# Kernel tuning notes

Hardware: AMD Instinct MI355X
Metric: run time of the kernel (lower is better)

The kernel has to match this reference:

```python
import jax, jax.numpy as jnp
import numpy as np

NUM_HEADS = 16

def setup_inputs() -> dict:
    key = jax.random.key(0)
    ks = jax.random.split(key, 5)
    b, c, w, h = 2, 1024, 48, 48
    sc = 0.02
    return {
        "x": jax.random.normal(ks[0], (b, c, w, h), jnp.float32),
        "Wqkv": jax.random.normal(ks[1], (3 * c, c), jnp.float32) * sc,
        "bqkv": jax.random.normal(ks[2], (3 * c,), jnp.float32) * sc,
        "Wo": jax.random.normal(ks[3], (c, c), jnp.float32) * sc,
        "bo": jax.random.normal(ks[4], (c,), jnp.float32) * sc,
    }

def reference(x, Wqkv, bqkv, Wo, bo):
    b, c, w, h = x.shape
    n = NUM_HEADS
    hd = c // n
    s = w * h
    # [b,c,w,h] -> tokens [b, s, c]
    xs = x.transpose(0, 2, 3, 1).reshape(b, s, c)
    qkv = xs @ Wqkv.T + bqkv                       # [b, s, 3c]
    # rearrange 'b s (three n hd) -> three b n s hd'
    qkv = qkv.reshape(b, s, 3, n, hd).transpose(2, 0, 3, 1, 4)
    q, k, v = qkv[0], qkv[1], qkv[2]               # [b, n, s, hd]
    score = jnp.einsum('bnqh,bnkh->bnqk', q, k) / jnp.sqrt(jnp.float32(hd))
    # module uses a soft causal mask: subtract 10000 above the diagonal
    mask = 10000.0 * jnp.triu(jnp.ones((s, s), dtype=score.dtype), k=1)
    attn = jax.nn.softmax(score - mask, axis=-1)   # [b, n, s, s]
    z = jnp.einsum('bnqk,bnkh->bqnh', attn, v).reshape(b, s, c)
    out = z @ Wo.T + bo                            # [b, s, c]
    return out.reshape(b, w, h, c).transpose(0, 3, 1, 2)
```

## Files before the change

### kernel.cpp

```cpp
#include <hip/hip_runtime.h>

typedef __bf16 bf16;
typedef __bf16 bf16x8 __attribute__((ext_vector_type(8)));
typedef float floatx4 __attribute__((ext_vector_type(4)));

static constexpr int S = 2304;
static constexpr int C = 1024;
static constexpr int NHEAD = 16;
static constexpr int HDIM = 64;
static constexpr int BATCH = 2;
static constexpr float QSCALE = 0.18033688011112042f;
static constexpr int QSPLIT = 18;
static constexpr int NACC = S - QSPLIT * 64;

__global__ __launch_bounds__(256) void k_zero(float4* __restrict__ p, int n4) {
  int i = blockIdx.x * 256 + threadIdx.x;
  if (i < n4) p[i] = float4{0.f, 0.f, 0.f, 0.f};
}

__global__ __launch_bounds__(256) void k_convert(const float* __restrict__ src,
                                                 bf16* __restrict__ dst, int n8) {
  int i = blockIdx.x * 256 + threadIdx.x;
  if (i >= n8) return;
  float4 a = *(const float4*)(src + (size_t)i * 8);
  float4 b = *(const float4*)(src + (size_t)i * 8 + 4);
  bf16x8 o;
  o[0] = (bf16)a.x; o[1] = (bf16)a.y; o[2] = (bf16)a.z; o[3] = (bf16)a.w;
  o[4] = (bf16)b.x; o[5] = (bf16)b.y; o[6] = (bf16)b.z; o[7] = (bf16)b.w;
  *(bf16x8*)(dst + (size_t)i * 8) = o;
}

__global__ __launch_bounds__(256) void k_transpose(const float* __restrict__ x,
                                                   bf16* __restrict__ xs) {
  __shared__ bf16 T[64 * 72];
  int c0 = blockIdx.x * 64, t0 = blockIdx.y * 64, b = blockIdx.z;
  int tid = threadIdx.x;
  const float* xb = x + (size_t)b * C * S;
#pragma unroll
  for (int it = 0; it < 4; ++it) {
    int idx = it * 256 + tid;
    int rc = idx >> 4, t4 = idx & 15;
    float4 v = *(const float4*)(xb + (size_t)(c0 + rc) * S + t0 + t4 * 4);
    T[(t4 * 4 + 0) * 72 + rc] = (bf16)v.x;
    T[(t4 * 4 + 1) * 72 + rc] = (bf16)v.y;
    T[(t4 * 4 + 2) * 72 + rc] = (bf16)v.z;
    T[(t4 * 4 + 3) * 72 + rc] = (bf16)v.w;
  }
  __syncthreads();
  bf16* xsb = xs + (size_t)b * S * C;
#pragma unroll
  for (int it = 0; it < 2; ++it) {
    int idx = it * 256 + tid;
    int rt = idx >> 3, c8 = idx & 7;
    bf16x8 v;
#pragma unroll
    for (int i = 0; i < 8; ++i) v[i] = T[rt * 72 + c8 * 8 + i];
    *(bf16x8*)(xsb + (size_t)(t0 + rt) * C + c0 + c8 * 8) = v;
  }
}

__device__ __forceinline__ void g2l16(const bf16* g, bf16* l) {
  __builtin_amdgcn_global_load_lds(
      (const __attribute__((address_space(1))) void*)g,
      (__attribute__((address_space(3))) void*)l, 16, 0, 0);
}

template <int EPI>
__global__ __launch_bounds__(256) void k_gemm_bt(const bf16* __restrict__ A,
                                                 const bf16* __restrict__ Bt,
                                                 const float* __restrict__ bias,
                                                 bf16* __restrict__ q,
                                                 bf16* __restrict__ k,
                                                 bf16* __restrict__ v,
                                                 float* __restrict__ outf) {
  constexpr int K = C;
  __shared__ bf16 As[128 * 64];
  __shared__ bf16 Bs[128 * 64];
  int tid = threadIdx.x;
  int w = tid >> 6, lane = tid & 63, ln = lane & 15, quad = lane >> 4;
  int m0 = blockIdx.y * 128, n0 = blockIdx.x * 128;
  int moff = (w >> 1) * 64, noff = (w & 1) * 64;
  floatx4 acc[4][4] = {};

  int sr[4], sc[4];
#pragma unroll
  for (int it = 0; it < 4; ++it) {
    int L = (it * 4 + w) * 64 + lane;
    sr[it] = L >> 3;
    sc[it] = (L & 7) ^ (sr[it] & 7);
  }

  for (int k0 = 0; k0 < K; k0 += 64) {
    __syncthreads();
#pragma unroll
    for (int it = 0; it < 4; ++it) {
      int cb = (it * 4 + w) * 64;
      g2l16(A + (size_t)(m0 + sr[it]) * K + k0 + sc[it] * 8, As + cb * 8);
      g2l16(Bt + (size_t)(n0 + sr[it]) * K + k0 + sc[it] * 8, Bs + cb * 8);
    }
    __syncthreads();
#pragma unroll
    for (int t = 0; t < 2; ++t) {
      bf16x8 af[4], bfr[4];
#pragma unroll
      for (int i = 0; i < 4; ++i) {
        int ra = moff + i * 16 + ln;
        af[i]  = *(const bf16x8*)(As + ra * 64 + (((t * 4 + quad) ^ (ra & 7))) * 8);
        int rb = noff + i * 16 + ln;
        bfr[i] = *(const bf16x8*)(Bs + rb * 64 + (((t * 4 + quad) ^ (rb & 7))) * 8);
      }
#pragma unroll
      for (int im = 0; im < 4; ++im)
#pragma unroll
        for (int in = 0; in < 4; ++in)
          acc[im][in] = __builtin_amdgcn_mfma_f32_16x16x32_bf16(
              af[im], bfr[in], acc[im][in], 0, 0, 0);
    }
  }

  int bidx = (m0 >= S) ? 1 : 0;
  if (EPI == 0) {
#pragma unroll
    for (int in = 0; in < 4; ++in) {
      int j = n0 + noff + in * 16 + ln;
      float bv = bias[j];
      int three = j >> 10;
      int head = (j >> 6) & 15;
      int hdi = j & 63;
#pragma unroll
      for (int im = 0; im < 4; ++im) {
        int mbase = m0 + moff + im * 16 + quad * 4;
        int tb = mbase - bidx * S;
        if (three == 2) {
          union { ushort4 u; bf16 h[4]; } P;
#pragma unroll
          for (int r = 0; r < 4; ++r) P.h[r] = (bf16)(acc[im][in][r] + bv);
          *(ushort4*)(v + ((size_t)(bidx * NHEAD + head) * HDIM + hdi) * S + tb) = P.u;
        } else if (three == 0) {
          bf16* dst = q + ((size_t)(bidx * NHEAD + head) * S + tb) * HDIM + hdi;
#pragma unroll
          for (int r = 0; r < 4; ++r)
            dst[(size_t)r * HDIM] = (bf16)((acc[im][in][r] + bv) * QSCALE);
        } else {
          bf16* dst = k + ((size_t)(bidx * NHEAD + head) * S + tb) * HDIM + hdi;
#pragma unroll
          for (int r = 0; r < 4; ++r) dst[(size_t)r * HDIM] = (bf16)(acc[im][in][r] + bv);
        }
      }
    }
  } else {
#pragma unroll
    for (int in = 0; in < 4; ++in) {
      int co = n0 + noff + in * 16 + ln;
      float bv = bias[co];
#pragma unroll
      for (int im = 0; im < 4; ++im) {
        int mbase = m0 + moff + im * 16 + quad * 4;
        int tb = mbase - bidx * S;
        float4 st;
        st.x = acc[im][in][0] + bv;
        st.y = acc[im][in][1] + bv;
        st.z = acc[im][in][2] + bv;
        st.w = acc[im][in][3] + bv;
        *(float4*)(outf + ((size_t)bidx * C + co) * S + tb) = st;
      }
    }
  }
}

__global__ __launch_bounds__(512) void k_attn_part(const bf16* __restrict__ Qg,
                                                   const bf16* __restrict__ Kg,
                                                   const bf16* __restrict__ Vtg,
                                                   bf16* __restrict__ z,
                                                   float* __restrict__ Oacc,
                                                   float* __restrict__ Lacc) {
  __shared__ bf16 Ks[2][64 * 64];
  __shared__ bf16 Vs[2][64 * 64];
  __shared__ bf16 Pt[128 * 64];
  int i = blockIdx.x;
  int xcd = i & 7, j = i >> 3;
  int grp = j / 27, r = j % 27;
  int bh = xcd + 8 * grp;
  int qi, lo, hi;
  bool single = (r >= 18);
  if (!single) {
    qi = 17 - (r >> 1);
    lo = (r & 1) * (qi + 1);
    hi = lo + qi + 1;
  } else {
    qi = 26 - r;
    lo = 0;
    hi = 2 * qi + 2;
  }
  int b = bh >> 4, h = bh & 15;
  int tid = threadIdx.x;
  int w = tid >> 6, lane = tid & 63, ln = lane & 15, quad = lane >> 4;
  int q0 = qi * 128;
  int qw = q0 + w * 16;
  int qg = qw + ln;
  int ktd = qw >> 6;

  const bf16* kb = Kg + (size_t)bh * S * HDIM;
  const bf16* vb = Vtg + (size_t)bh * HDIM * S;

  int s_row = tid >> 3, s_c8 = tid & 7;
  int s_cs = s_c8 ^ (s_row & 7);
  size_t kOff = (size_t)s_row * HDIM + s_cs * 8;
  size_t vOff = (size_t)s_row * S + s_cs * 8;

  const bf16* qb = Qg + ((size_t)bh * S + qg) * HDIM + quad * 8;
  bf16x8 qf0 = *(const bf16x8*)qb;
  bf16x8 qf1 = *(const bf16x8*)(qb + 32);

  float lsum = 0.f;
  floatx4 o_acc[4] = {};

  int prow = w * 16 + ln;
  int psw = ln & 7;
  bf16* ptw = Pt + prow * 64 + (quad & 1) * 4;
  const bf16* ptr = Pt + prow * 64;
  int qloc = (w & 3) * 16 + ln;

  const bf16* kb0 = kb + (size_t)lo * 64 * HDIM;
  const bf16* vb0 = vb + (size_t)lo * 64;
  g2l16(kb0 + kOff, Ks[0] + tid * 8);
  g2l16(vb0 + vOff, Vs[0] + tid * 8);

  const bf16* kbn = kb0 + (size_t)64 * HDIM;
  const bf16* vbn = vb0 + 64;

#pragma unroll 1
  for (int kt = lo; kt < hi; ++kt) {
    int cur = (kt - lo) & 1;
    __syncthreads();

    if (kt + 1 < hi) {
      g2l16(kbn + kOff, Ks[1 - cur] + tid * 8);
      g2l16(vbn + vOff, Vs[1 - cur] + tid * 8);
      kbn += (size_t)64 * HDIM;
      vbn += 64;
    }

    if (kt > ktd) continue;

    floatx4 s_acc[4] = {};
#pragma unroll
    for (int kf = 0; kf < 4; ++kf) {
      int row = kf * 16 + ln;
      int sw = row & 7;
      bf16x8 k0 = *(const bf16x8*)(Ks[cur] + row * 64 + (sw ^ quad) * 8);
      bf16x8 k1 = *(const bf16x8*)(Ks[cur] + row * 64 + ((4 ^ sw) ^ quad) * 8);
      s_acc[kf] = __builtin_amdgcn_mfma_f32_16x16x32_bf16(k0, qf0, s_acc[kf], 0, 0, 0);
      s_acc[kf] = __builtin_amdgcn_mfma_f32_16x16x32_bf16(k1, qf1, s_acc[kf], 0, 0, 0);
    }

    if (kt < ktd) {
#pragma unroll
      for (int kf = 0; kf < 4; ++kf) {
        union { ushort4 u; bf16 hh[4]; } P;
#pragma unroll
        for (int rr = 0; rr < 4; ++rr) {
          float pv = exp2f(s_acc[kf][rr]);
          lsum += pv;
          P.hh[rr] = (bf16)pv;
        }
        *(ushort4*)(ptw + (((kf * 2 + (quad >> 1)) ^ psw)) * 8) = P.u;
      }
    } else {
#pragma unroll
      for (int kf = 0; kf < 4; ++kf) {
        union { ushort4 u; bf16 hh[4]; } P;
#pragma unroll
        for (int rr = 0; rr < 4; ++rr) {
          int kl = kf * 16 + quad * 4 + rr;
          float pv = (kl > qloc) ? 0.f : exp2f(s_acc[kf][rr]);
          lsum += pv;
          P.hh[rr] = (bf16)pv;
        }
        *(ushort4*)(ptw + (((kf * 2 + (quad >> 1)) ^ psw)) * 8) = P.u;
      }
    }

#pragma unroll
    for (int t = 0; t < 2; ++t) {
      bf16x8 pf = *(const bf16x8*)(ptr + (((t * 4 + quad) ^ psw)) * 8);
#pragma unroll
      for (int hf = 0; hf < 4; ++hf) {
        int row = hf * 16 + ln;
        int sw = row & 7;
        bf16x8 vf = *(const bf16x8*)(Vs[cur] + row * 64 + (((t * 4 + quad) ^ sw)) * 8);
        o_acc[hf] = __builtin_amdgcn_mfma_f32_16x16x32_bf16(vf, pf, o_acc[hf], 0, 0, 0);
      }
    }
  }

  lsum += __shfl_xor(lsum, 16);
  lsum += __shfl_xor(lsum, 32);

  if (single) {
    float inv = 1.f / lsum;
    bf16* dst = z + ((size_t)b * S + qg) * C + h * HDIM + quad * 4;
#pragma unroll
    for (int hf = 0; hf < 4; ++hf) {
      union { ushort4 u; bf16 hh[4]; } P;
#pragma unroll
      for (int rr = 0; rr < 4; ++rr) P.hh[rr] = (bf16)(o_acc[hf][rr] * inv);
      *(ushort4*)(dst + hf * 16) = P.u;
    }
  } else {
    int qa = qg - QSPLIT * 64;
    if (lane < 16) atomicAdd(&Lacc[bh * NACC + qa], lsum);
#pragma unroll
    for (int hf = 0; hf < 4; ++hf)
#pragma unroll
      for (int rr = 0; rr < 4; ++rr)
        atomicAdd(&Oacc[((size_t)bh * 64 + hf * 16 + quad * 4 + rr) * NACC + qa],
                  o_acc[hf][rr]);
  }
}

__global__ __launch_bounds__(256) void k_norm(const float* __restrict__ Oacc,
                                              const float* __restrict__ Lacc,
                                              bf16* __restrict__ z) {
  __shared__ float T[64 * 65];
  int qt = blockIdx.x, bh = blockIdx.y;
  int b = bh >> 4, h = bh & 15;
  int qrel0 = qt * 64;
  int q0 = QSPLIT * 64 + qrel0;
  int tid = threadIdx.x;
  int q4 = (tid & 15) * 4, hd0 = tid >> 4;
  float4 lv = *(const float4*)(Lacc + bh * NACC + qrel0 + q4);
  float inv0 = 1.f / lv.x, inv1 = 1.f / lv.y, inv2 = 1.f / lv.z, inv3 = 1.f / lv.w;
#pragma unroll
  for (int hf = 0; hf < 4; ++hf) {
    int hd = hf * 16 + hd0;
    float4 v = *(const float4*)(Oacc + ((size_t)bh * 64 + hd) * NACC + qrel0 + q4);
    T[(q4 + 0) * 65 + hd] = v.x * inv0;
    T[(q4 + 1) * 65 + hd] = v.y * inv1;
    T[(q4 + 2) * 65 + hd] = v.z * inv2;
    T[(q4 + 3) * 65 + hd] = v.w * inv3;
  }
  __syncthreads();
#pragma unroll
  for (int it = 0; it < 2; ++it) {
    int idx = it * 256 + tid;
    int qq = idx >> 3, c8 = idx & 7;
    bf16x8 o;
#pragma unroll
    for (int k = 0; k < 8; ++k) o[k] = (bf16)T[qq * 65 + c8 * 8 + k];
    *(bf16x8*)(z + ((size_t)b * S + q0 + qq) * C + h * HDIM + c8 * 8) = o;
  }
}

extern "C" void kernel_launch(void* const* d_in, const int* in_sizes, int n_in,
                              void* d_out, int out_size, void* d_ws, size_t ws_size,
                              hipStream_t stream) {
  const float* x    = (const float*)d_in[0];
  const float* Wqkv = (const float*)d_in[1];
  const float* bqkv = (const float*)d_in[2];
  const float* Wo   = (const float*)d_in[3];
  const float* bo   = (const float*)d_in[4];
  float* out = (float*)d_out;

  bf16* ws = (bf16*)d_ws;
  const size_t tok = (size_t)BATCH * S * C;
  bf16* xs   = ws;
  bf16* Qg   = ws + tok;
  bf16* Kg   = ws + 2 * tok;
  bf16* Vtg  = ws + 3 * tok;
  bf16* Wqb  = ws + 4 * tok;
  bf16* Wob  = Wqb + (size_t)3 * C * C;
  float* Oacc = (float*)(Wob + (size_t)C * C);
  float* Lacc = Oacc + (size_t)32 * 64 * NACC;
  bf16* z    = xs;

  k_zero<<<2340, 256, 0, stream>>>((float4*)Oacc, 599040);
  k_convert<<<(3 * C * C / 8 + 255) / 256, 256, 0, stream>>>(Wqkv, Wqb, 3 * C * C / 8);
  k_convert<<<(C * C / 8 + 255) / 256, 256, 0, stream>>>(Wo, Wob, C * C / 8);
  k_transpose<<<dim3(C / 64, S / 64, BATCH), 256, 0, stream>>>(x, xs);
  k_gemm_bt<0><<<dim3(3 * C / 128, BATCH * S / 128), 256, 0, stream>>>(
      xs, Wqb, bqkv, Qg, Kg, Vtg, nullptr);
  k_attn_part<<<dim3(864), 512, 0, stream>>>(Qg, Kg, Vtg, z, Oacc, Lacc);
  k_norm<<<dim3(18, 32), 256, 0, stream>>>(Oacc, Lacc, z);
  k_gemm_bt<1><<<dim3(C / 128, BATCH * S / 128), 256, 0, stream>>>(
      z, Wob, bo, nullptr, nullptr, nullptr, out);
}
```

Before: 216.4 us.

## Switch attention to 32x32 MFMA with register-resident P via permlane swap

Rewrites the attention inner loop to use 32x32x16 bf16 MFMAs with 4 waves of 32 query rows each instead of 8 waves of 16 rows. The softmax probabilities are packed with v_cvt_pk_bf16_f32 and rearranged across lanes with v_permlane32_swap, so P goes straight into the PV MFMA operand without the LDS round trip and its shared buffer. It also adds s_setprio around the MFMA phases. The cost is higher register pressure per wave and fewer waves per block to hide latency.

```diff
diff --git a/kernel.cpp b/kernel.cpp
--- a/kernel.cpp
+++ b/kernel.cpp
@@ -3,6 +3,7 @@
 typedef __bf16 bf16;
 typedef __bf16 bf16x8 __attribute__((ext_vector_type(8)));
 typedef float floatx4 __attribute__((ext_vector_type(4)));
+typedef float floatx16 __attribute__((ext_vector_type(16)));
 
 static constexpr int S = 2304;
 static constexpr int C = 1024;
@@ -63,6 +64,16 @@
   __builtin_amdgcn_global_load_lds(
       (const __attribute__((address_space(1))) void*)g,
       (__attribute__((address_space(3))) void*)l, 16, 0, 0);
+}
+
+__device__ __forceinline__ unsigned cvtpk(float a, float b) {
+  unsigned r;
+  asm("v_cvt_pk_bf16_f32 %0, %1, %2" : "=v"(r) : "v"(a), "v"(b));
+  return r;
+}
+
+__device__ __forceinline__ void pl32(unsigned& a, unsigned& b) {
+  asm("v_permlane32_swap_b32 %0, %1" : "+v"(a), "+v"(b));
 }
 
 template <int EPI>
@@ -168,7 +179,7 @@
   }
 }
 
-__global__ __launch_bounds__(512) void k_attn_part(const bf16* __restrict__ Qg,
+__global__ __launch_bounds__(256) void k_attn_part(const bf16* __restrict__ Qg,
                                                    const bf16* __restrict__ Kg,
                                                    const bf16* __restrict__ Vtg,
                                                    bf16* __restrict__ z,
@@ -176,7 +187,6 @@
                                                    float* __restrict__ Lacc) {
   __shared__ bf16 Ks[2][64 * 64];
   __shared__ bf16 Vs[2][64 * 64];
-  __shared__ bf16 Pt[128 * 64];
   int i = blockIdx.x;
   int xcd = i & 7, j = i >> 3;
   int grp = j / 27, r = j % 27;
@@ -194,40 +204,42 @@
   }
   int b = bh >> 4, h = bh & 15;
   int tid = threadIdx.x;
-  int w = tid >> 6, lane = tid & 63, ln = lane & 15, quad = lane >> 4;
+  int w = tid >> 6, lane = tid & 63;
+  int ql = lane & 31, hw = lane >> 5;
   int q0 = qi * 128;
-  int qw = q0 + w * 16;
-  int qg = qw + ln;
+  int qw = q0 + w * 32;
+  int qg = qw + ql;
   int ktd = qw >> 6;
 
   const bf16* kb = Kg + (size_t)bh * S * HDIM;
   const bf16* vb = Vtg + (size_t)bh * HDIM * S;
 
-  int s_row = tid >> 3, s_c8 = tid & 7;
-  int s_cs = s_c8 ^ (s_row & 7);
-  size_t kOff = (size_t)s_row * HDIM + s_cs * 8;
-  size_t vOff = (size_t)s_row * S + s_cs * 8;
-
-  const bf16* qb = Qg + ((size_t)bh * S + qg) * HDIM + quad * 8;
-  bf16x8 qf0 = *(const bf16x8*)qb;
-  bf16x8 qf1 = *(const bf16x8*)(qb + 32);
+  int s_row = tid >> 3;
+  int s_c8 = (tid & 7) ^ (s_row & 7);
+  size_t kOff1 = (size_t)s_row * HDIM + s_c8 * 8;
+  size_t kOff2 = kOff1 + (size_t)32 * HDIM;
+  size_t vOff1 = (size_t)s_row * S + s_c8 * 8;
+  size_t vOff2 = vOff1 + (size_t)32 * S;
+
+  const bf16* qb = Qg + ((size_t)bh * S + qg) * HDIM + hw * 8;
+  bf16x8 qf[4];
+#pragma unroll
+  for (int c = 0; c < 4; ++c) qf[c] = *(const bf16x8*)(qb + c * 16);
 
   float lsum = 0.f;
-  floatx4 o_acc[4] = {};
-
-  int prow = w * 16 + ln;
-  int psw = ln & 7;
-  bf16* ptw = Pt + prow * 64 + (quad & 1) * 4;
-  const bf16* ptr = Pt + prow * 64;
-  int qloc = (w & 3) * 16 + ln;
+  floatx16 o0 = {}, o1 = {};
 
   const bf16* kb0 = kb + (size_t)lo * 64 * HDIM;
   const bf16* vb0 = vb + (size_t)lo * 64;
-  g2l16(kb0 + kOff, Ks[0] + tid * 8);
-  g2l16(vb0 + vOff, Vs[0] + tid * 8);
+  g2l16(kb0 + kOff1, Ks[0] + tid * 8);
+  g2l16(kb0 + kOff2, Ks[0] + (256 + tid) * 8);
+  g2l16(vb0 + vOff1, Vs[0] + tid * 8);
+  g2l16(vb0 + vOff2, Vs[0] + (256 + tid) * 8);
 
   const bf16* kbn = kb0 + (size_t)64 * HDIM;
   const bf16* vbn = vb0 + 64;
+
+  int qsw = ql & 7;
 
 #pragma unroll 1
   for (int kt = lo; kt < hi; ++kt) {
@@ -235,87 +247,112 @@
     __syncthreads();
 
     if (kt + 1 < hi) {
-      g2l16(kbn + kOff, Ks[1 - cur] + tid * 8);
-      g2l16(vbn + vOff, Vs[1 - cur] + tid * 8);
+      bf16* kd = Ks[1 - cur];
+      bf16* vd = Vs[1 - cur];
+      g2l16(kbn + kOff1, kd + tid * 8);
+      g2l16(kbn + kOff2, kd + (256 + tid) * 8);
+      g2l16(vbn + vOff1, vd + tid * 8);
+      g2l16(vbn + vOff2, vd + (256 + tid) * 8);
       kbn += (size_t)64 * HDIM;
       vbn += 64;
     }
 
     if (kt > ktd) continue;
-
-    floatx4 s_acc[4] = {};
-#pragma unroll
-    for (int kf = 0; kf < 4; ++kf) {
-      int row = kf * 16 + ln;
-      int sw = row & 7;
-      bf16x8 k0 = *(const bf16x8*)(Ks[cur] + row * 64 + (sw ^ quad) * 8);
-      bf16x8 k1 = *(const bf16x8*)(Ks[cur] + row * 64 + ((4 ^ sw) ^ quad) * 8);
-      s_acc[kf] = __builtin_amdgcn_mfma_f32_16x16x32_bf16(k0, qf0, s_acc[kf], 0, 0, 0);
-      s_acc[kf] = __builtin_amdgcn_mfma_f32_16x16x32_bf16(k1, qf1, s_acc[kf], 0, 0, 0);
-    }
-
-    if (kt < ktd) {
-#pragma unroll
-      for (int kf = 0; kf < 4; ++kf) {
-        union { ushort4 u; bf16 hh[4]; } P;
-#pragma unroll
-        for (int rr = 0; rr < 4; ++rr) {
-          float pv = exp2f(s_acc[kf][rr]);
-          lsum += pv;
-          P.hh[rr] = (bf16)pv;
-        }
-        *(ushort4*)(ptw + (((kf * 2 + (quad >> 1)) ^ psw)) * 8) = P.u;
+    bool diag = (kt == ktd);
+
+    const bf16* ksb = Ks[cur];
+    const bf16* vsb = Vs[cur];
+
+    floatx16 sa0 = {}, sa1 = {};
+    __builtin_amdgcn_s_setprio(1);
+#pragma unroll
+    for (int c = 0; c < 4; ++c) {
+      int c8 = ((2 * c + hw) ^ qsw) * 8;
+      bf16x8 k0 = *(const bf16x8*)(ksb + ql * 64 + c8);
+      bf16x8 k1 = *(const bf16x8*)(ksb + (32 + ql) * 64 + c8);
+      sa0 = __builtin_amdgcn_mfma_f32_32x32x16_bf16(k0, qf[c], sa0, 0, 0, 0);
+      sa1 = __builtin_amdgcn_mfma_f32_32x32x16_bf16(k1, qf[c], sa1, 0, 0, 0);
+    }
+    __builtin_amdgcn_s_setprio(0);
+
+    unsigned pk0[8], pk1[8];
+    if (!diag) {
+#pragma unroll
+      for (int t = 0; t < 8; ++t) {
+        float a = exp2f(sa0[2 * t]), c2 = exp2f(sa0[2 * t + 1]);
+        float d = exp2f(sa1[2 * t]), e = exp2f(sa1[2 * t + 1]);
+        lsum += (a + c2) + (d + e);
+        pk0[t] = cvtpk(a, c2);
+        pk1[t] = cvtpk(d, e);
       }
     } else {
-#pragma unroll
-      for (int kf = 0; kf < 4; ++kf) {
-        union { ushort4 u; bf16 hh[4]; } P;
-#pragma unroll
-        for (int rr = 0; rr < 4; ++rr) {
-          int kl = kf * 16 + quad * 4 + rr;
-          float pv = (kl > qloc) ? 0.f : exp2f(s_acc[kf][rr]);
-          lsum += pv;
-          P.hh[rr] = (bf16)pv;
-        }
-        *(ushort4*)(ptw + (((kf * 2 + (quad >> 1)) ^ psw)) * 8) = P.u;
-      }
-    }
-
-#pragma unroll
-    for (int t = 0; t < 2; ++t) {
-      bf16x8 pf = *(const bf16x8*)(ptr + (((t * 4 + quad) ^ psw)) * 8);
-#pragma unroll
-      for (int hf = 0; hf < 4; ++hf) {
-        int row = hf * 16 + ln;
-        int sw = row & 7;
-        bf16x8 vf = *(const bf16x8*)(Vs[cur] + row * 64 + (((t * 4 + quad) ^ sw)) * 8);
-        o_acc[hf] = __builtin_amdgcn_mfma_f32_16x16x32_bf16(vf, pf, o_acc[hf], 0, 0, 0);
-      }
-    }
-  }
-
-  lsum += __shfl_xor(lsum, 16);
+      int qd = qg - kt * 64;
+#pragma unroll
+      for (int t = 0; t < 8; ++t) {
+        int r0 = 2 * t, r1 = 2 * t + 1;
+        int k0l = (r0 & 3) + 8 * (r0 >> 2) + 4 * hw;
+        int k1l = (r1 & 3) + 8 * (r1 >> 2) + 4 * hw;
+        float a = (k0l > qd) ? 0.f : exp2f(sa0[r0]);
+        float c2 = (k1l > qd) ? 0.f : exp2f(sa0[r1]);
+        float d = (32 + k0l > qd) ? 0.f : exp2f(sa1[r0]);
+        float e = (32 + k1l > qd) ? 0.f : exp2f(sa1[r1]);
+        lsum += (a + c2) + (d + e);
+        pk0[t] = cvtpk(a, c2);
+        pk1[t] = cvtpk(d, e);
+      }
+    }
+
+    __builtin_amdgcn_s_setprio(1);
+#pragma unroll
+    for (int ktc = 0; ktc < 4; ++ktc) {
+      unsigned d0, d1, d2, d3;
+      if (ktc == 0)      { d0 = pk0[0]; d1 = pk0[1]; d2 = pk0[2]; d3 = pk0[3]; }
+      else if (ktc == 1) { d0 = pk0[4]; d1 = pk0[5]; d2 = pk0[6]; d3 = pk0[7]; }
+      else if (ktc == 2) { d0 = pk1[0]; d1 = pk1[1]; d2 = pk1[2]; d3 = pk1[3]; }
+      else               { d0 = pk1[4]; d1 = pk1[5]; d2 = pk1[6]; d3 = pk1[7]; }
+      pl32(d0, d2);
+      pl32(d1, d3);
+      union { unsigned u[4]; bf16x8 v; } pf;
+      pf.u[0] = d0; pf.u[1] = d1; pf.u[2] = d2; pf.u[3] = d3;
+      int c8 = ((2 * ktc + hw) ^ qsw) * 8;
+      bf16x8 v0 = *(const bf16x8*)(vsb + ql * 64 + c8);
+      bf16x8 v1 = *(const bf16x8*)(vsb + (32 + ql) * 64 + c8);
+      o0 = __builtin_amdgcn_mfma_f32_32x32x16_bf16(v0, pf.v, o0, 0, 0, 0);
+      o1 = __builtin_amdgcn_mfma_f32_32x32x16_bf16(v1, pf.v, o1, 0, 0, 0);
+    }
+    __builtin_amdgcn_s_setprio(0);
+  }
+
   lsum += __shfl_xor(lsum, 32);
 
   if (single) {
     float inv = 1.f / lsum;
-    bf16* dst = z + ((size_t)b * S + qg) * C + h * HDIM + quad * 4;
-#pragma unroll
-    for (int hf = 0; hf < 4; ++hf) {
-      union { ushort4 u; bf16 hh[4]; } P;
-#pragma unroll
-      for (int rr = 0; rr < 4; ++rr) P.hh[rr] = (bf16)(o_acc[hf][rr] * inv);
-      *(ushort4*)(dst + hf * 16) = P.u;
+    bf16* dst = z + ((size_t)b * S + qg) * C + h * HDIM + 4 * hw;
+#pragma unroll
+    for (int hdblk = 0; hdblk < 2; ++hdblk) {
+#pragma unroll
+      for (int rg = 0; rg < 4; ++rg) {
+        union { ushort4 u; bf16 hh[4]; } P;
+#pragma unroll
+        for (int jj = 0; jj < 4; ++jj) {
+          float ov = hdblk ? o1[rg * 4 + jj] : o0[rg * 4 + jj];
+          P.hh[jj] = (bf16)(ov * inv);
+        }
+        *(ushort4*)(dst + hdblk * 32 + rg * 8) = P.u;
+      }
     }
   } else {
     int qa = qg - QSPLIT * 64;
-    if (lane < 16) atomicAdd(&Lacc[bh * NACC + qa], lsum);
-#pragma unroll
-    for (int hf = 0; hf < 4; ++hf)
-#pragma unroll
-      for (int rr = 0; rr < 4; ++rr)
-        atomicAdd(&Oacc[((size_t)bh * 64 + hf * 16 + quad * 4 + rr) * NACC + qa],
-                  o_acc[hf][rr]);
+    if (hw == 0) atomicAdd(&Lacc[bh * NACC + qa], lsum);
+#pragma unroll
+    for (int hdblk = 0; hdblk < 2; ++hdblk) {
+#pragma unroll
+      for (int rr = 0; rr < 16; ++rr) {
+        int hd = hdblk * 32 + (rr & 3) + 8 * (rr >> 2) + 4 * hw;
+        float ov = hdblk ? o1[rr] : o0[rr];
+        atomicAdd(&Oacc[((size_t)bh * 64 + hd) * NACC + qa], ov);
+      }
+    }
   }
 }
 
@@ -380,7 +417,7 @@
   k_transpose<<<dim3(C / 64, S / 64, BATCH), 256, 0, stream>>>(x, xs);
   k_gemm_bt<0><<<dim3(3 * C / 128, BATCH * S / 128), 256, 0, stream>>>(
       xs, Wqb, bqkv, Qg, Kg, Vtg, nullptr);
-  k_attn_part<<<dim3(864), 512, 0, stream>>>(Qg, Kg, Vtg, z, Oacc, Lacc);
+  k_attn_part<<<dim3(864), 256, 0, stream>>>(Qg, Kg, Vtg, z, Oacc, Lacc);
   k_norm<<<dim3(18, 32), 256, 0, stream>>>(Oacc, Lacc, z);
   k_gemm_bt<1><<<dim3(C / 128, BATCH * S / 128), 256, 0, stream>>>(
       z, Wob, bo, nullptr, nullptr, nullptr, out);
```

After: 224.8 us. +3.9%, slower.
